# Kernel tuning notes

Hardware: AMD Instinct MI355X
Metric: run time of the kernel (lower is better)

Reference implementation:

```python
import jax, jax.numpy as jnp
import numpy as np

B, CQ, CKV, E = 8, 256, 256, 256
H, W = 64, 64
HP, WP = 32, 32


def setup_inputs() -> dict:
    key = jax.random.key(0)
    ks = jax.random.split(key, 6)
    C = jax.random.normal(ks[0], (B, CQ, H, W), dtype=jnp.float32)
    P = jax.random.normal(ks[1], (B, CKV, HP, WP), dtype=jnp.float32)
    # 1x1 conv weights, kaiming-ish scale; stored as [out_ch, in_ch]
    theta_w = jax.random.normal(ks[2], (E, CQ), dtype=jnp.float32) * (1.0 / np.sqrt(CQ))
    phi_w = jax.random.normal(ks[3], (E, CKV), dtype=jnp.float32) * (1.0 / np.sqrt(CKV))
    g_w = jax.random.normal(ks[4], (E, CKV), dtype=jnp.float32) * (1.0 / np.sqrt(CKV))
    out_w = jax.random.normal(ks[5], (CQ, E), dtype=jnp.float32) * (1.0 / np.sqrt(E))
    return {"C": C, "P": P, "theta_w": theta_w, "phi_w": phi_w, "g_w": g_w, "out_w": out_w}


def reference(C, P, theta_w, phi_w, g_w, out_w):
    b, _, h, w = C.shape
    e = theta_w.shape[0]
    # 1x1 convs are channel GEMMs
    theta_C = jnp.einsum('bchw,ec->behw', C, theta_w).reshape(b, e, h * w)   # [B,E,Nq]
    phi_P = jnp.einsum('bchw,ec->behw', P, phi_w).reshape(b, e, -1)          # [B,E,Nkv]
    g_P = jnp.einsum('bchw,ec->behw', P, g_w).reshape(b, e, -1)              # [B,E,Nkv]
    attn = jnp.einsum('ben,bem->bnm', theta_C, phi_P) / (e ** 0.5)           # [B,Nq,Nkv]
    attn = jax.nn.softmax(attn, axis=-1)
    out = jnp.einsum('bem,bnm->ben', g_P, attn).reshape(b, e, h, w)          # [B,E,H,W]
    out = jnp.einsum('behw,ce->bchw', out, out_w)                            # [B,CQ,H,W]
    return jnp.concatenate([C, out], axis=1)
```

## Files before the change

kernel.cpp:

```cpp
#include <hip/hip_runtime.h>


typedef __attribute__((ext_vector_type(8))) short short8;
typedef __attribute__((ext_vector_type(16))) float f32x16;
typedef unsigned short ushort_t;

__device__ __forceinline__ unsigned short f2bf(float f) {
    unsigned int u = __float_as_uint(f);
    u += 0x7FFFu + ((u >> 16) & 1u);
    return (unsigned short)(u >> 16);
}
__device__ __forceinline__ unsigned int pack2bf(float a, float b) {
    return (unsigned int)f2bf(a) | ((unsigned int)f2bf(b) << 16);
}
__device__ __forceinline__ void gload16(const ushort_t* g, ushort_t* l) {
    __builtin_amdgcn_global_load_lds(
        (const __attribute__((address_space(1))) unsigned int*)g,
        (__attribute__((address_space(3))) unsigned int*)l, 16, 0, 0);
}
__device__ __forceinline__ f32x16 zero16() {
    f32x16 z;
#pragma unroll
    for (int i = 0; i < 16; ++i) z[i] = 0.f;
    return z;
}

__global__ __launch_bounds__(256) void prep_w(const float* __restrict__ thw,
                                              const float* __restrict__ phw,
                                              const float* __restrict__ ow,
                                              const float* __restrict__ gw,
                                              ushort_t* __restrict__ thc,
                                              ushort_t* __restrict__ phc,
                                              ushort_t* __restrict__ w2c) {
    int blk = blockIdx.x;
    int t = threadIdx.x;
    if (blk < 512) {
        int which = blk >> 8;
        int e = blk & 255, c = t;
        const float* src = which ? phw : thw;
        ushort_t* dst = which ? phc : thc;
        int idx = ((((e >> 5) * 16 + (c >> 4)) * 64 + ((c >> 3) & 1) * 32 + (e & 31)) << 3) + (c & 7);
        dst[idx] = f2bf(src[e * 256 + c]);
    } else {
        int c0 = (blk - 512) * 8;
        float acc[8] = {};
        for (int e = 0; e < 256; ++e) {
            float g = gw[e * 256 + t];
#pragma unroll
            for (int i = 0; i < 8; ++i) acc[i] += ow[(c0 + i) * 256 + e] * g;
        }
#pragma unroll
        for (int i = 0; i < 8; ++i) {
            int c = c0 + i, k = t;
            int idx = ((((c >> 5) * 16 + (k >> 4)) * 64 + ((k >> 3) & 1) * 32 + (c & 31)) << 3) + (k & 7);
            w2c[idx] = f2bf(acc[i]);
        }
    }
}

__global__ __launch_bounds__(256, 2) void proj_all(const ushort_t* __restrict__ thc,
                                                   const ushort_t* __restrict__ phc,
                                                   const ushort_t* __restrict__ w2c,
                                                   const float* __restrict__ C,
                                                   const float* __restrict__ P,
                                                   ushort_t* __restrict__ thetaA,
                                                   ushort_t* __restrict__ phiA,
                                                   ushort_t* __restrict__ gVx) {
    __shared__ float Xs[256][68];
    int blk = blockIdx.x;
    int tid = threadIdx.x, lane = tid & 63, wid = tid >> 6;
    int l31 = lane & 31, lh = lane >> 5;
    const int wq = wid & 1, we = wid >> 1;

    int role, b, nt, N;
    const ushort_t* Wc;
    const float* Xg;
    ushort_t* outp;
    float scale = 1.f;
    if (blk < 512) {
        role = 0; b = blk & 7; nt = blk >> 3;
        Wc = thc; Xg = C + (size_t)b * 1048576; outp = thetaA + (size_t)b * 1048576;
        N = 4096; scale = 1.4426950408889634f / 16.0f;
    } else if (blk < 640) {
        int r = blk - 512; role = 1; b = r & 7; nt = r >> 3;
        Wc = phc; Xg = P + (size_t)b * 262144; outp = phiA + (size_t)b * 262144;
        N = 1024;
    } else {
        int r = blk - 640; role = 2; b = r & 7; nt = r >> 3;
        Wc = w2c; Xg = P + (size_t)b * 262144; outp = gVx + (size_t)b * 262144;
        N = 1024;
    }

    {
        const float* Xb = Xg + nt * 64;
#pragma unroll
        for (int i = 0; i < 16; ++i) {
            int idx = i * 256 + tid;
            int row = idx >> 4, c4 = (idx & 15) * 4;
            *(float4*)&Xs[row][c4] = *(const float4*)(Xb + (size_t)row * N + c4);
        }
    }
    __syncthreads();

    const int n0 = nt * 64 + wq * 32;
    const int ncr = (n0 >> 5) * 16;
    const int q = wq * 32 + l31;

    f32x16 o[4];
#pragma unroll
    for (int f = 0; f < 4; ++f) o[f] = zero16();

#pragma unroll
    for (int ks = 0; ks < 16; ++ks) {
        const int cb = ks * 16 + lh * 8;
        union PW { unsigned int u[4]; short8 v; } xw;
#pragma unroll
        for (int j = 0; j < 4; ++j)
            xw.u[j] = pack2bf(Xs[cb + 2 * j][q], Xs[cb + 2 * j + 1][q]);
#pragma unroll
        for (int f2 = 0; f2 < 4; ++f2) {
            int f = we * 4 + f2;
            short8 wf = *(const short8*)(Wc + ((size_t)(f * 16 + ks) * 64 + lane) * 8);
            o[f2] = __builtin_amdgcn_mfma_f32_32x32x16_bf16(wf, xw.v, o[f2], 0, 0, 0);
        }
    }

    if (role < 2) {
#pragma unroll
        for (int f2 = 0; f2 < 4; ++f2) {
            int f = we * 4 + f2;
#pragma unroll
            for (int rq = 0; rq < 4; ++rq) {
                uint2 st;
                st.x = pack2bf(o[f2][4 * rq + 0] * scale, o[f2][4 * rq + 1] * scale);
                st.y = pack2bf(o[f2][4 * rq + 2] * scale, o[f2][4 * rq + 3] * scale);
                size_t addr = ((size_t)(ncr + f * 2 + (rq >> 1)) * 64 + l31 + 32 * (rq & 1)) * 8 + 4 * lh;
                *(uint2*)(outp + addr) = st;
            }
        }
    } else {
        int kvq = (n0 >> 4) + (l31 >> 4);
        int lhw = 32 * ((l31 >> 3) & 1);
        int kl = l31 & 7;
#pragma unroll
        for (int f2 = 0; f2 < 4; ++f2) {
            int f = we * 4 + f2;
#pragma unroll
            for (int r2 = 0; r2 < 16; ++r2) {
                int crow = (r2 & 3) + 8 * (r2 >> 2) + 4 * lh;
                size_t addr = ((size_t)(f * 64 + kvq) * 64 + crow + lhw) * 8 + kl;
                outp[addr] = f2bf(o[f2][r2]);
            }
        }
    }
}

__global__ __launch_bounds__(512, 2) void attn11(const ushort_t* __restrict__ thetaA,
                                                 const ushort_t* __restrict__ phiA,
                                                 const ushort_t* __restrict__ gVx,
                                                 const float* __restrict__ Cf,
                                                 float* __restrict__ out) {
    const int b = blockIdx.x & 7, qt = blockIdx.x >> 3;
    const int tid = threadIdx.x, lane = tid & 63, wid = tid >> 6;
    const int l31 = lane & 31, lh = lane >> 5;
    const int qg = wid & 3, z = wid >> 2;

    __shared__ __align__(16) ushort_t smem[65536];
    __shared__ __align__(16) ushort_t Pl[8192];
    __shared__ float rlS[2][4][32];

    const ushort_t* thA = thetaA + (size_t)b * 1048576;
    const ushort_t* phA = phiA + (size_t)b * 262144;
    const ushort_t* gVb = gVx + (size_t)b * 262144;

    auto stage = [&](int j, int d) {
        if (wid < 4) {
            const ushort_t* src = phA + (size_t)j * 16384 + (size_t)wid * 4096 + lane * 8;
            ushort_t* dst = smem + d * 16384 + wid * 4096;
#pragma unroll
            for (int i = 0; i < 8; ++i) gload16(src + i * 512, dst + i * 512);
        } else {
            int w = wid - 4;
#pragma unroll
            for (int q2 = 0; q2 < 2; ++q2) {
                int f = w * 2 + q2;
#pragma unroll
                for (int jj = 0; jj < 4; ++jj) {
                    const ushort_t* src = gVb + ((size_t)(f * 64 + j * 4 + jj) * 64 + lane) * 8;
                    ushort_t* dst = smem + 32768 + d * 16384 + f * 2048 + jj * 512;
                    gload16(src, dst);
                }
            }
        }
    };

    stage(0, 0);

    short8 qf[16];
    {
        const int qcr = (qt * 4 + qg) * 16;
#pragma unroll
        for (int ks = 0; ks < 16; ++ks)
            qf[ks] = *(const short8*)(thA + ((size_t)(qcr + ks) * 64 + lane) * 8);
    }

    f32x16 o[4];
#pragma unroll
    for (int f = 0; f < 4; ++f) o[f] = zero16();
    float rl = 0.f;

    const size_t cbase = (size_t)b * 1048576 + (size_t)qt * 128 + (size_t)l31 * 4;
    const size_t dofs = (size_t)b * 1048576;
    size_t cpo = 0;
    float4 cpv;

    for (int it = 0; it < 16; ++it) {
        asm volatile("s_waitcnt vmcnt(0)" ::: "memory");
        __builtin_amdgcn_s_barrier();
        __builtin_amdgcn_sched_barrier(0);
        if (it < 15) stage(it + 1, (it + 1) & 1);

        if (it > 0) *(float4*)(out + cpo + dofs) = cpv;
        cpo = cbase + (size_t)(it * 16 + 2 * wid + lh) * 4096;
        cpv = *(const float4*)(Cf + cpo);

        const ushort_t* Kb = smem + (it & 1) * 16384 + z * 8192;
        const ushort_t* Vb = smem + 32768 + (it & 1) * 16384 + z * 8192;

        f32x16 s = zero16();
        __builtin_amdgcn_s_setprio(1);
#pragma unroll
        for (int ks = 0; ks < 16; ++ks) {
            short8 kf = *(const short8*)(Kb + (size_t)ks * 512 + lane * 8);
            s = __builtin_amdgcn_mfma_f32_32x32x16_bf16(kf, qf[ks], s, 0, 0, 0);
        }
        __builtin_amdgcn_s_setprio(0);

#pragma unroll
        for (int r = 0; r < 16; ++r) s[r] = __builtin_amdgcn_exp2f(s[r]);
        float t0 = (s[0] + s[1]) + (s[2] + s[3]);
        float t1 = (s[4] + s[5]) + (s[6] + s[7]);
        float t2 = (s[8] + s[9]) + (s[10] + s[11]);
        float t3 = (s[12] + s[13]) + (s[14] + s[15]);
        float ps = (t0 + t1) + (t2 + t3);
        ps += __shfl_xor(ps, 32);
        rl += ps;

        unsigned int a0 = pack2bf(s[0], s[1]),   b0 = pack2bf(s[4], s[5]);
        unsigned int a1 = pack2bf(s[2], s[3]),   b1 = pack2bf(s[6], s[7]);
        unsigned int a2 = pack2bf(s[8], s[9]),   b2 = pack2bf(s[12], s[13]);
        unsigned int a3 = pack2bf(s[10], s[11]), b3 = pack2bf(s[14], s[15]);
        asm volatile("v_permlane32_swap_b32 %0, %1" : "+v"(a0), "+v"(b0));
        asm volatile("v_permlane32_swap_b32 %0, %1" : "+v"(a1), "+v"(b1));
        asm volatile("v_permlane32_swap_b32 %0, %1" : "+v"(a2), "+v"(b2));
        asm volatile("v_permlane32_swap_b32 %0, %1" : "+v"(a3), "+v"(b3));
        union PW { unsigned int u[4]; short8 v; };
        PW pw0, pw1;
        pw0.u[0] = a0; pw0.u[1] = a1; pw0.u[2] = b0; pw0.u[3] = b1;
        pw1.u[0] = a2; pw1.u[1] = a3; pw1.u[2] = b2; pw1.u[3] = b3;

        *(short8*)(Pl + ((size_t)(qg * 4 + 2 * z + 0) * 64 + lane) * 8) = pw0.v;
        *(short8*)(Pl + ((size_t)(qg * 4 + 2 * z + 1) * 64 + lane) * 8) = pw1.v;
        asm volatile("s_waitcnt lgkmcnt(0)" ::: "memory");
        __builtin_amdgcn_s_barrier();

        __builtin_amdgcn_s_setprio(1);
#pragma unroll
        for (int j = 0; j < 4; ++j) {
            short8 pf = *(const short8*)(Pl + ((size_t)(qg * 4 + j) * 64 + lane) * 8);
#pragma unroll
            for (int fl = 0; fl < 4; ++fl) {
                short8 vf = *(const short8*)(Vb + (size_t)fl * 2048 + j * 512 + lane * 8);
                o[fl] = __builtin_amdgcn_mfma_f32_32x32x16_bf16(vf, pf, o[fl], 0, 0, 0);
            }
        }
        __builtin_amdgcn_s_setprio(0);
    }

    *(float4*)(out + cpo + dofs) = cpv;

    if (lane < 32) rlS[z][qg][l31] = rl;
    __syncthreads();
    float inv = 1.f / (rlS[0][qg][l31] + rlS[1][qg][l31]);
    float* ob = out + (size_t)b * 2097152 + (size_t)256 * 4096 + qt * 128 + qg * 32 + l31;
#pragma unroll
    for (int fl = 0; fl < 4; ++fl) {
#pragma unroll
        for (int r = 0; r < 16; ++r) {
            int e = z * 128 + fl * 32 + (r & 3) + 8 * (r >> 2) + 4 * lh;
            ob[(size_t)e * 4096] = o[fl][r] * inv;
        }
    }
}


extern "C" void kernel_launch(void* const* d_in, const int* in_sizes, int n_in,
                              void* d_out, int out_size, void* d_ws, size_t ws_size,
                              hipStream_t stream) {
    const float* C       = (const float*)d_in[0];
    const float* P       = (const float*)d_in[1];
    const float* theta_w = (const float*)d_in[2];
    const float* phi_w   = (const float*)d_in[3];
    const float* g_w     = (const float*)d_in[4];
    const float* out_w   = (const float*)d_in[5];
    float* out = (float*)d_out;

    ushort_t* ws = (ushort_t*)d_ws;
    ushort_t* thetaA = ws;
    ushort_t* phiA   = ws + 8388608;
    ushort_t* gVx    = ws + 10485760;
    ushort_t* thWc   = ws + 12582912;
    ushort_t* phWc   = ws + 12648448;
    ushort_t* w2c    = ws + 12713984;

    prep_w<<<544, 256, 0, stream>>>(theta_w, phi_w, out_w, g_w, thWc, phWc, w2c);
    proj_all<<<768, 256, 0, stream>>>(thWc, phWc, w2c, C, P, thetaA, phiA, gVx);
    attn11<<<256, 512, 0, stream>>>(thetaA, phiA, gVx, C, out);
}
```

Before: 113.4 us.

## Software-pipeline attention loop: overlap next QK^T MFMAs with current PV MFMAs

Restructures the attention main loop so the QK^T score MFMAs for the next KV tile are interleaved with the PV MFMAs of the current tile. K is prefetched two tiles ahead and V one tile ahead, with separate staging lambdas and adjusted vmcnt waits. The aim is to hide the exp/softmax and LDS round-trip latency behind independent matrix work. In exchange it raises register pressure from the extra accumulator and adds a barrier per iteration; the vmcnt(1) accounting is also fragile.

After: 110.1 us. 1.03x faster.

```diff
diff --git a/kernel.cpp b/kernel.cpp
--- a/kernel.cpp
+++ b/kernel.cpp
@@ -155,7 +155,7 @@
     }
 }
 
-__global__ __launch_bounds__(512, 2) void attn11(const ushort_t* __restrict__ thetaA,
+__global__ __launch_bounds__(512, 2) void attn12(const ushort_t* __restrict__ thetaA,
                                                  const ushort_t* __restrict__ phiA,
                                                  const ushort_t* __restrict__ gVx,
                                                  const float* __restrict__ Cf,
@@ -173,13 +173,16 @@
     const ushort_t* phA = phiA + (size_t)b * 262144;
     const ushort_t* gVb = gVx + (size_t)b * 262144;
 
-    auto stage = [&](int j, int d) {
+    auto stageK = [&](int j) {
         if (wid < 4) {
             const ushort_t* src = phA + (size_t)j * 16384 + (size_t)wid * 4096 + lane * 8;
-            ushort_t* dst = smem + d * 16384 + wid * 4096;
+            ushort_t* dst = smem + (j & 1) * 16384 + wid * 4096;
 #pragma unroll
             for (int i = 0; i < 8; ++i) gload16(src + i * 512, dst + i * 512);
-        } else {
+        }
+    };
+    auto stageV = [&](int j) {
+        if (wid >= 4) {
             int w = wid - 4;
 #pragma unroll
             for (int q2 = 0; q2 < 2; ++q2) {
@@ -187,14 +190,14 @@
 #pragma unroll
                 for (int jj = 0; jj < 4; ++jj) {
                     const ushort_t* src = gVb + ((size_t)(f * 64 + j * 4 + jj) * 64 + lane) * 8;
-                    ushort_t* dst = smem + 32768 + d * 16384 + f * 2048 + jj * 512;
+                    ushort_t* dst = smem + 32768 + (j & 1) * 16384 + f * 2048 + jj * 512;
                     gload16(src, dst);
                 }
             }
         }
     };
 
-    stage(0, 0);
+    stageK(0); stageV(0);
 
     short8 qf[16];
     {
@@ -202,6 +205,21 @@
 #pragma unroll
         for (int ks = 0; ks < 16; ++ks)
             qf[ks] = *(const short8*)(thA + ((size_t)(qcr + ks) * 64 + lane) * 8);
+    }
+
+    asm volatile("s_waitcnt vmcnt(0)" ::: "memory");
+    __builtin_amdgcn_s_barrier();
+    __builtin_amdgcn_sched_barrier(0);
+    stageK(1);
+
+    f32x16 s = zero16();
+    {
+        const ushort_t* Kb = smem + z * 8192;
+#pragma unroll
+        for (int ks = 0; ks < 16; ++ks) {
+            short8 kf = *(const short8*)(Kb + (size_t)ks * 512 + lane * 8);
+            s = __builtin_amdgcn_mfma_f32_32x32x16_bf16(kf, qf[ks], s, 0, 0, 0);
+        }
     }
 
     f32x16 o[4];
@@ -215,27 +233,6 @@
     float4 cpv;
 
     for (int it = 0; it < 16; ++it) {
-        asm volatile("s_waitcnt vmcnt(0)" ::: "memory");
-        __builtin_amdgcn_s_barrier();
-        __builtin_amdgcn_sched_barrier(0);
-        if (it < 15) stage(it + 1, (it + 1) & 1);
-
-        if (it > 0) *(float4*)(out + cpo + dofs) = cpv;
-        cpo = cbase + (size_t)(it * 16 + 2 * wid + lh) * 4096;
-        cpv = *(const float4*)(Cf + cpo);
-
-        const ushort_t* Kb = smem + (it & 1) * 16384 + z * 8192;
-        const ushort_t* Vb = smem + 32768 + (it & 1) * 16384 + z * 8192;
-
-        f32x16 s = zero16();
-        __builtin_amdgcn_s_setprio(1);
-#pragma unroll
-        for (int ks = 0; ks < 16; ++ks) {
-            short8 kf = *(const short8*)(Kb + (size_t)ks * 512 + lane * 8);
-            s = __builtin_amdgcn_mfma_f32_32x32x16_bf16(kf, qf[ks], s, 0, 0, 0);
-        }
-        __builtin_amdgcn_s_setprio(0);
-
 #pragma unroll
         for (int r = 0; r < 16; ++r) s[r] = __builtin_amdgcn_exp2f(s[r]);
         float t0 = (s[0] + s[1]) + (s[2] + s[3]);
@@ -258,23 +255,54 @@
         PW pw0, pw1;
         pw0.u[0] = a0; pw0.u[1] = a1; pw0.u[2] = b0; pw0.u[3] = b1;
         pw1.u[0] = a2; pw1.u[1] = a3; pw1.u[2] = b2; pw1.u[3] = b3;
-
         *(short8*)(Pl + ((size_t)(qg * 4 + 2 * z + 0) * 64 + lane) * 8) = pw0.v;
         *(short8*)(Pl + ((size_t)(qg * 4 + 2 * z + 1) * 64 + lane) * 8) = pw1.v;
+
+        if (it == 0) asm volatile("s_waitcnt vmcnt(0)" ::: "memory");
+        else         asm volatile("s_waitcnt vmcnt(1)" ::: "memory");
         asm volatile("s_waitcnt lgkmcnt(0)" ::: "memory");
         __builtin_amdgcn_s_barrier();
-
+        __builtin_amdgcn_sched_barrier(0);
+
+        if (it > 0) *(float4*)(out + cpo + dofs) = cpv;
+        if (it < 14) stageK(it + 2);
+        if (it < 15) stageV(it + 1);
+        __builtin_amdgcn_sched_barrier(0);
+        cpo = cbase + (size_t)(it * 16 + 2 * wid + lh) * 4096;
+        cpv = *(const float4*)(Cf + cpo);
+
+        const ushort_t* Vb = smem + 32768 + (it & 1) * 16384 + z * 8192;
+        const ushort_t* Kb = smem + ((it + 1) & 1) * 16384 + z * 8192;
         __builtin_amdgcn_s_setprio(1);
-#pragma unroll
-        for (int j = 0; j < 4; ++j) {
-            short8 pf = *(const short8*)(Pl + ((size_t)(qg * 4 + j) * 64 + lane) * 8);
-#pragma unroll
-            for (int fl = 0; fl < 4; ++fl) {
-                short8 vf = *(const short8*)(Vb + (size_t)fl * 2048 + j * 512 + lane * 8);
-                o[fl] = __builtin_amdgcn_mfma_f32_32x32x16_bf16(vf, pf, o[fl], 0, 0, 0);
+        if (it < 15) {
+            f32x16 sn = zero16();
+#pragma unroll
+            for (int j = 0; j < 4; ++j) {
+                short8 pf = *(const short8*)(Pl + ((size_t)(qg * 4 + j) * 64 + lane) * 8);
+#pragma unroll
+                for (int fl = 0; fl < 4; ++fl) {
+                    short8 vf = *(const short8*)(Vb + (size_t)fl * 2048 + j * 512 + lane * 8);
+                    o[fl] = __builtin_amdgcn_mfma_f32_32x32x16_bf16(vf, pf, o[fl], 0, 0, 0);
+                    int ks = j * 4 + fl;
+                    short8 kf = *(const short8*)(Kb + (size_t)ks * 512 + lane * 8);
+                    sn = __builtin_amdgcn_mfma_f32_32x32x16_bf16(kf, qf[ks], sn, 0, 0, 0);
+                }
+            }
+            s = sn;
+        } else {
+#pragma unroll
+            for (int j = 0; j < 4; ++j) {
+                short8 pf = *(const short8*)(Pl + ((size_t)(qg * 4 + j) * 64 + lane) * 8);
+#pragma unroll
+                for (int fl = 0; fl < 4; ++fl) {
+                    short8 vf = *(const short8*)(Vb + (size_t)fl * 2048 + j * 512 + lane * 8);
+                    o[fl] = __builtin_amdgcn_mfma_f32_32x32x16_bf16(vf, pf, o[fl], 0, 0, 0);
+                }
             }
         }
         __builtin_amdgcn_s_setprio(0);
+        __builtin_amdgcn_sched_barrier(0);
+        __builtin_amdgcn_s_barrier();
     }
 
     *(float4*)(out + cpo + dofs) = cpv;
@@ -315,5 +343,5 @@
 
     prep_w<<<544, 256, 0, stream>>>(theta_w, phi_w, out_w, g_w, thWc, phWc, w2c);
     proj_all<<<768, 256, 0, stream>>>(thWc, phWc, w2c, C, P, thetaA, phiA, gVx);
-    attn11<<<256, 512, 0, stream>>>(thetaA, phiA, gVx, C, out);
-}
+    attn12<<<256, 512, 0, stream>>>(thetaA, phiA, gVx, C, out);
+}
```
